# Kernel optimization log

Measured on AMD Instinct MI355X. Metric: run time of the kernel, lower is better.

Reference implementation:

```python
import jax, jax.numpy as jnp
import numpy as np

NEG_INF = -1.0e9  # matches the module's explicit -1e9 masking constant


def setup_inputs() -> dict:
    key = jax.random.key(0)
    B, T, D = 8, 2048, 1024
    x = jax.random.normal(key, (B, T, D), dtype=jnp.float32)
    return {"x": x}


def reference(x):
    # x: [B, T, D]
    T = x.shape[1]
    # raw QK^T scores: [B, T, T]
    scores = jnp.einsum('btd,bsd->bts', x, x)
    # torch.tril(scores, -1) + torch.triu(ones*-1e9, 0):
    # keep strictly-lower entries, set diagonal and upper to -1e9.
    strict_lower = jnp.tril(jnp.ones((T, T), dtype=bool), k=-1)
    scores = jnp.where(strict_lower, scores, jnp.float32(NEG_INF))
    # NOTE: row 0 is all -1e9 -> softmax yields uniform 1/T (faithful to the torch code).
    att_weights = jax.nn.softmax(scores, axis=-1)  # [B, T, T]
    att_vec = jnp.einsum('bts,bsd->btd', att_weights, x)  # [B, T, D]
    return att_vec, att_weights
```

## Files before the change

### kernel.cpp

```cpp
#include <hip/hip_runtime.h>

#define B_ 8
#define T_ 2048
#define D_ 1024

typedef __attribute__((ext_vector_type(8))) short bf16x8;
typedef __attribute__((ext_vector_type(8))) _Float16 f16x8;
typedef __attribute__((ext_vector_type(4))) float f32x4;
typedef __attribute__((ext_vector_type(8))) unsigned short u16x8;
typedef __attribute__((ext_vector_type(4))) unsigned short u16x4;

__device__ __forceinline__ unsigned short f2bf(float f) {
  union { float f; unsigned u; } v; v.f = f;
  unsigned r = v.u + 0x7FFFu + ((v.u >> 16) & 1u);
  return (unsigned short)(r >> 16);
}
__device__ __forceinline__ float bf2f(unsigned short h) {
  union { unsigned u; float f; } v; v.u = ((unsigned)h) << 16; return v.f;
}
__device__ __forceinline__ unsigned short f2h(float f) {
  union { _Float16 h; unsigned short u; } v; v.h = (_Float16)f; return v.u;
}

__device__ __forceinline__ void gl2lds16(const void* g, void* l) {
  __builtin_amdgcn_global_load_lds(
      (__attribute__((address_space(1))) void*)g,
      (__attribute__((address_space(3))) void*)l, 16, 0, 0);
}

__global__ __launch_bounds__(256) void prep_kernel(
    const float* __restrict__ x,
    unsigned short* __restrict__ xh, unsigned short* __restrict__ xl,
    unsigned short* __restrict__ xth) {
  const int b = blockIdx.z;
  const int t0 = blockIdx.y << 6;
  const int d0 = blockIdx.x << 6;
  __shared__ unsigned short tf[64][68];
  const int tid = threadIdx.x;
  const int row = tid & 63, cq = tid >> 6;
  const size_t xoff = ((size_t)b * T_ + t0 + row) * D_ + d0;
#pragma unroll
  for (int c = 0; c < 4; ++c) {
    const int col = (cq << 4) + (c << 2);
    const float4 v = *(const float4*)(x + xoff + col);
    const unsigned short h0 = f2bf(v.x), h1 = f2bf(v.y), h2 = f2bf(v.z), h3 = f2bf(v.w);
    const unsigned short l0 = f2bf(v.x - bf2f(h0)), l1 = f2bf(v.y - bf2f(h1));
    const unsigned short l2 = f2bf(v.z - bf2f(h2)), l3 = f2bf(v.w - bf2f(h3));
    u16x4 hv = {h0, h1, h2, h3}, lv = {l0, l1, l2, l3};
    *(u16x4*)(xh + xoff + col) = hv;
    *(u16x4*)(xl + xoff + col) = lv;
    tf[col + 0][row] = f2h(v.x); tf[col + 1][row] = f2h(v.y);
    tf[col + 2][row] = f2h(v.z); tf[col + 3][row] = f2h(v.w);
  }
  __syncthreads();
  const size_t toff = ((size_t)b * D_ + d0 + row) * T_ + t0;
#pragma unroll
  for (int c = 0; c < 4; ++c) {
    const int col = (cq << 4) + (c << 2);
    *(u16x4*)(xth + toff + col) = *(const u16x4*)&tf[row][col];
  }
}

__global__ __launch_bounds__(256, 4) void scores_mfma(
    const unsigned short* __restrict__ xh, const unsigned short* __restrict__ xl,
    float* __restrict__ w) {
  const int id = blockIdx.x;
  const int sid = ((id & 7) * 136) + (id >> 3);
  const int b = sid / 136;
  const int L = sid - b * 136;
  int tt = (int)((sqrtf(8.f * (float)L + 1.f) - 1.f) * 0.5f);
  while (((tt + 1) * (tt + 2) >> 1) <= L) ++tt;
  while (((tt * (tt + 1)) >> 1) > L) --tt;
  const int ts = L - ((tt * (tt + 1)) >> 1);

  const int t0 = tt << 7, s0 = ts << 7;
  __shared__ unsigned short Ah[128 * 32];
  __shared__ unsigned short Al[128 * 32];
  __shared__ unsigned short Bh[128 * 32];
  __shared__ unsigned short Bl[128 * 32];
  const int tid = threadIdx.x;
  const int lane = tid & 63, wv = tid >> 6;
  const int wr = (wv >> 1) << 6, wc = (wv & 1) << 6;
  const int quad = lane >> 4, r16 = lane & 15;
  const int swz = ((quad ^ (r16 & 3) ^ ((r16 >> 2) & 1)) << 3);
  const size_t xb = (size_t)b * T_ * D_;

  f32x4 acc[4][4];
#pragma unroll
  for (int i = 0; i < 4; ++i)
#pragma unroll
    for (int j = 0; j < 4; ++j) acc[i][j] = (f32x4){0.f, 0.f, 0.f, 0.f};

  for (int k0 = 0; k0 < D_; k0 += 32) {
    __syncthreads();
#pragma unroll
    for (int i = 0; i < 2; ++i) {
      const int cc = (wv << 7) + (i << 6) + lane;
      const int row = cc >> 2, q = cc & 3;
      const int gq = q ^ (row & 3) ^ ((row >> 2) & 1);
      const int ldsoff = (((wv << 7) + (i << 6)) << 3);
      const size_t ga = xb + (size_t)(t0 + row) * D_ + k0 + (gq << 3);
      const size_t gb = xb + (size_t)(s0 + row) * D_ + k0 + (gq << 3);
      gl2lds16(xh + ga, &Ah[ldsoff]);
      gl2lds16(xl + ga, &Al[ldsoff]);
      gl2lds16(xh + gb, &Bh[ldsoff]);
      gl2lds16(xl + gb, &Bl[ldsoff]);
    }
    __syncthreads();
    bf16x8 ah[4], al[4];
#pragma unroll
    for (int i = 0; i < 4; ++i) {
      const int ra = ((wr + (i << 4) + r16) << 5) + swz;
      ah[i] = *(const bf16x8*)&Ah[ra];
      al[i] = *(const bf16x8*)&Al[ra];
    }
#pragma unroll
    for (int j = 0; j < 4; ++j) {
      const int rb = ((wc + (j << 4) + r16) << 5) + swz;
      const bf16x8 bhj = *(const bf16x8*)&Bh[rb];
      const bf16x8 blj = *(const bf16x8*)&Bl[rb];
#pragma unroll
      for (int i = 0; i < 4; ++i)
        acc[i][j] = __builtin_amdgcn_mfma_f32_16x16x32_bf16(ah[i], bhj, acc[i][j], 0, 0, 0);
#pragma unroll
      for (int i = 0; i < 4; ++i)
        acc[i][j] = __builtin_amdgcn_mfma_f32_16x16x32_bf16(ah[i], blj, acc[i][j], 0, 0, 0);
#pragma unroll
      for (int i = 0; i < 4; ++i)
        acc[i][j] = __builtin_amdgcn_mfma_f32_16x16x32_bf16(al[i], bhj, acc[i][j], 0, 0, 0);
    }
  }

  float* wb = w + (size_t)b * T_ * T_;
#pragma unroll
  for (int i = 0; i < 4; ++i)
#pragma unroll
    for (int j = 0; j < 4; ++j) {
      const int rr = t0 + wr + (i << 4) + (quad << 2);
      const int cc = s0 + wc + (j << 4) + r16;
#pragma unroll
      for (int rg = 0; rg < 4; ++rg)
        wb[(size_t)(rr + rg) * T_ + cc] = acc[i][j][rg];
    }
}

template <bool EMIT>
__global__ __launch_bounds__(256) void softmax_kernel(float* __restrict__ w,
                                                      unsigned short* __restrict__ wf) {
  const int row = (blockIdx.x << 2) + (threadIdx.x >> 6);
  const int t = row & (T_ - 1);
  const int lane = threadIdx.x & 63;
  float* wr = w + (size_t)row * T_;
  unsigned short* wfr = wf + (size_t)row * T_;

  if (t == 0) {
    const float u = 1.0f / 2048.0f;
#pragma unroll
    for (int k = 0; k < 32; ++k) {
      wr[lane + (k << 6)] = u;
      if (EMIT && k < 2) wfr[lane + (k << 6)] = 0;
    }
    return;
  }

  const int kmax = ((t >> 7) + 1) << 1;
  float v[32];
  float m = -3.0e38f;
#pragma unroll
  for (int k = 0; k < 32; ++k) {
    const int s = lane + (k << 6);
    float val = -1.0e30f;
    if (s < t) val = wr[s];
    v[k] = val;
    m = fmaxf(m, val);
  }
#pragma unroll
  for (int off = 32; off; off >>= 1) m = fmaxf(m, __shfl_xor(m, off));

  float l = 0.f;
#pragma unroll
  for (int k = 0; k < 32; ++k) {
    v[k] = __expf(v[k] - m);
    l += v[k];
  }
#pragma unroll
  for (int off = 32; off; off >>= 1) l += __shfl_xor(l, off);
  const float inv = 1.0f / l;

#pragma unroll
  for (int k = 0; k < 32; ++k) {
    const float o = v[k] * inv;
    const int s = lane + (k << 6);
    wr[s] = o;
    if (EMIT && k < kmax) wfr[s] = f2h(o);
  }
}

template <bool USE_WF16>
__global__ __launch_bounds__(256, 4) void av_mfma(
    const float* __restrict__ w, const unsigned short* __restrict__ wf,
    const unsigned short* __restrict__ xth, float* __restrict__ out) {
  const int xid = blockIdx.x;
  const int td = xid >> 4;
  const int ti = xid & 15;
  const int tt = (ti < 8) ? ti : (23 - ti);
  const int b = blockIdx.z;
  const int t0 = tt << 7, d0 = td << 7;
  __shared__ unsigned short Aw[128 * 32];
  __shared__ unsigned short Bx[128 * 32];
  const int tid = threadIdx.x;
  const int lane = tid & 63, wv = tid >> 6;
  const int wr = (wv >> 1) << 6, wc = (wv & 1) << 6;
  const int quad = lane >> 4, r16 = lane & 15;
  const int swz = ((quad ^ (r16 & 3) ^ ((r16 >> 2) & 1)) << 3);
  const size_t xtb = (size_t)b * D_ * T_;
  const size_t wbase = (size_t)b * T_ * T_;
  const int smax = t0 + 128;

  f32x4 acc[4][4];
#pragma unroll
  for (int i = 0; i < 4; ++i)
#pragma unroll
    for (int j = 0; j < 4; ++j) acc[i][j] = (f32x4){0.f, 0.f, 0.f, 0.f};

  for (int s0 = 0; s0 < smax; s0 += 32) {
    __syncthreads();
    if (USE_WF16) {
#pragma unroll
      for (int i = 0; i < 2; ++i) {
        const int cc = (wv << 7) + (i << 6) + lane;
        const int row = cc >> 2, q = cc & 3;
        const int gq = q ^ (row & 3) ^ ((row >> 2) & 1);
        const int ldsoff = (((wv << 7) + (i << 6)) << 3);
        gl2lds16(wf + wbase + (size_t)(t0 + row) * T_ + s0 + (gq << 3), &Aw[ldsoff]);
      }
    } else {
      const int row = tid >> 1, half = tid & 1;
      const float* g = w + wbase + (size_t)(t0 + row) * T_ + s0 + (half << 4);
      const float4 v0 = ((const float4*)g)[0];
      const float4 v1 = ((const float4*)g)[1];
      const float4 v2 = ((const float4*)g)[2];
      const float4 v3 = ((const float4*)g)[3];
      const int sw = (row & 3) ^ ((row >> 2) & 1);
      u16x8 p0 = {f2h(v0.x), f2h(v0.y), f2h(v0.z), f2h(v0.w),
                  f2h(v1.x), f2h(v1.y), f2h(v1.z), f2h(v1.w)};
      u16x8 p1 = {f2h(v2.x), f2h(v2.y), f2h(v2.z), f2h(v2.w),
                  f2h(v3.x), f2h(v3.y), f2h(v3.z), f2h(v3.w)};
      *(u16x8*)&Aw[(row << 5) + ((((half << 1) | 0) ^ sw) << 3)] = p0;
      *(u16x8*)&Aw[(row << 5) + ((((half << 1) | 1) ^ sw) << 3)] = p1;
    }
#pragma unroll
    for (int i = 0; i < 2; ++i) {
      const int cc = (wv << 7) + (i << 6) + lane;
      const int row = cc >> 2, q = cc & 3;
      const int gq = q ^ (row & 3) ^ ((row >> 2) & 1);
      const int ldsoff = (((wv << 7) + (i << 6)) << 3);
      gl2lds16(xth + xtb + (size_t)(d0 + row) * T_ + s0 + (gq << 3), &Bx[ldsoff]);
    }
    __syncthreads();
    f16x8 a[4];
#pragma unroll
    for (int i = 0; i < 4; ++i)
      a[i] = *(const f16x8*)&Aw[((wr + (i << 4) + r16) << 5) + swz];
#pragma unroll
    for (int j = 0; j < 4; ++j) {
      const f16x8 bbj = *(const f16x8*)&Bx[((wc + (j << 4) + r16) << 5) + swz];
#pragma unroll
      for (int i = 0; i < 4; ++i)
        acc[i][j] = __builtin_amdgcn_mfma_f32_16x16x32_f16(a[i], bbj, acc[i][j], 0, 0, 0);
    }
  }

  float* ob = out + (size_t)b * T_ * D_;
#pragma unroll
  for (int i = 0; i < 4; ++i)
#pragma unroll
    for (int j = 0; j < 4; ++j) {
      const int rr = t0 + wr + (i << 4) + (quad << 2);
      const int cc = d0 + wc + (j << 4) + r16;
#pragma unroll
      for (int rg = 0; rg < 4; ++rg)
        ob[(size_t)(rr + rg) * D_ + cc] = acc[i][j][rg];
    }
}

__global__ __launch_bounds__(256) void row0_partial(const float* __restrict__ x,
                                                    float* __restrict__ part) {
  const int tc = blockIdx.x, b = blockIdx.y;
  const int tid = threadIdx.x;
  const float* xb = x + ((size_t)b * T_ + (tc << 8)) * D_;
  float4 s = {0.f, 0.f, 0.f, 0.f};
#pragma unroll 4
  for (int r = 0; r < 256; ++r) {
    const float4 v = *(const float4*)(xb + (size_t)r * D_ + (tid << 2));
    s.x += v.x; s.y += v.y; s.z += v.z; s.w += v.w;
  }
  *(float4*)(part + ((size_t)((b << 3) + tc)) * D_ + (tid << 2)) = s;
}

__global__ __launch_bounds__(256) void row0_reduce(const float* __restrict__ part,
                                                   float* __restrict__ out) {
  const int b = blockIdx.x;
  const int tid = threadIdx.x;
  float4 s = {0.f, 0.f, 0.f, 0.f};
#pragma unroll
  for (int p = 0; p < 8; ++p) {
    const float4 v = *(const float4*)(part + ((size_t)((b << 3) + p)) * D_ + (tid << 2));
    s.x += v.x; s.y += v.y; s.z += v.z; s.w += v.w;
  }
  const float sc = 1.0f / 2048.0f;
  float4 o = {s.x * sc, s.y * sc, s.z * sc, s.w * sc};
  *(float4*)(out + (size_t)b * T_ * D_ + (tid << 2)) = o;
}

extern "C" void kernel_launch(void* const* d_in, const int* in_sizes, int n_in,
                              void* d_out, int out_size, void* d_ws, size_t ws_size,
                              hipStream_t stream) {
  const float* x = (const float*)d_in[0];
  float* att_vec = (float*)d_out;
  float* w = (float*)d_out + (size_t)B_ * T_ * D_;

  unsigned short* xh = (unsigned short*)att_vec;
  unsigned short* xl = xh + (size_t)B_ * T_ * D_;
  const size_t xthN = (size_t)B_ * D_ * T_;
  const size_t wfN = (size_t)B_ * T_ * T_;
  unsigned short* xth = (unsigned short*)d_ws;
  unsigned short* wf16 = xth + xthN;
  const size_t need = xthN * 2 + wfN * 2 + (size_t)64 * D_ * 4;
  const bool use_wf16 = (ws_size >= need);
  float* part = use_wf16 ? (float*)(wf16 + wfN) : (float*)(xth + xthN);

  prep_kernel<<<dim3(D_ / 64, T_ / 64, B_), 256, 0, stream>>>(x, xh, xl, xth);
  scores_mfma<<<dim3(8 * 136), 256, 0, stream>>>(xh, xl, w);
  if (use_wf16) {
    softmax_kernel<true><<<dim3(B_ * T_ / 4), 256, 0, stream>>>(w, wf16);
    av_mfma<true><<<dim3(128, 1, B_), 256, 0, stream>>>(w, wf16, xth, att_vec);
  } else {
    softmax_kernel<false><<<dim3(B_ * T_ / 4), 256, 0, stream>>>(w, wf16);
    av_mfma<false><<<dim3(128, 1, B_), 256, 0, stream>>>(w, wf16, xth, att_vec);
  }
  row0_partial<<<dim3(8, B_), 256, 0, stream>>>(x, part);
  row0_reduce<<<dim3(B_), 256, 0, stream>>>(part, att_vec);
}
```

Measured before the change: 538.5 us.

## Vectorize softmax, double AV k-tile to 64, and widen row0 reduction grid

The softmax kernel now loads and stores float4 and half4 vectors per lane instead of scalars, which reduces memory instruction count on the dominant weight traffic. The AV matmul k-tile is doubled from 32 to 64 with a new 8-way XOR swizzle, halving the number of barrier-separated iterations at the cost of more LDS per block. The row-0 mean reduction is split across 64 chunks per batch instead of 8 for more parallelism, and the workspace requirement grows to hold the extra partials.

```diff
diff --git a/kernel.cpp b/kernel.cpp
--- a/kernel.cpp
+++ b/kernel.cpp
@@ -155,44 +155,58 @@
 
   if (t == 0) {
     const float u = 1.0f / 2048.0f;
-#pragma unroll
-    for (int k = 0; k < 32; ++k) {
-      wr[lane + (k << 6)] = u;
-      if (EMIT && k < 2) wfr[lane + (k << 6)] = 0;
+    const float4 uv = {u, u, u, u};
+#pragma unroll
+    for (int k = 0; k < 8; ++k) *(float4*)&wr[(lane << 2) + (k << 8)] = uv;
+    if (EMIT && lane < 32) {
+      u16x4 z = {0, 0, 0, 0};
+      *(u16x4*)&wfr[lane << 2] = z;
     }
     return;
   }
 
-  const int kmax = ((t >> 7) + 1) << 1;
-  float v[32];
+  float4 v[8];
   float m = -3.0e38f;
 #pragma unroll
-  for (int k = 0; k < 32; ++k) {
-    const int s = lane + (k << 6);
-    float val = -1.0e30f;
-    if (s < t) val = wr[s];
+  for (int k = 0; k < 8; ++k) {
+    const int s = (lane << 2) + (k << 8);
+    float4 val = {-1.0e30f, -1.0e30f, -1.0e30f, -1.0e30f};
+    if (s < t) {
+      const float4 g = *(const float4*)&wr[s];
+      val.x = g.x;
+      val.y = (s + 1 < t) ? g.y : -1.0e30f;
+      val.z = (s + 2 < t) ? g.z : -1.0e30f;
+      val.w = (s + 3 < t) ? g.w : -1.0e30f;
+    }
     v[k] = val;
-    m = fmaxf(m, val);
+    m = fmaxf(m, fmaxf(fmaxf(val.x, val.y), fmaxf(val.z, val.w)));
   }
 #pragma unroll
   for (int off = 32; off; off >>= 1) m = fmaxf(m, __shfl_xor(m, off));
 
   float l = 0.f;
 #pragma unroll
-  for (int k = 0; k < 32; ++k) {
-    v[k] = __expf(v[k] - m);
-    l += v[k];
+  for (int k = 0; k < 8; ++k) {
+    v[k].x = __expf(v[k].x - m);
+    v[k].y = __expf(v[k].y - m);
+    v[k].z = __expf(v[k].z - m);
+    v[k].w = __expf(v[k].w - m);
+    l += (v[k].x + v[k].y) + (v[k].z + v[k].w);
   }
 #pragma unroll
   for (int off = 32; off; off >>= 1) l += __shfl_xor(l, off);
   const float inv = 1.0f / l;
 
-#pragma unroll
-  for (int k = 0; k < 32; ++k) {
-    const float o = v[k] * inv;
-    const int s = lane + (k << 6);
-    wr[s] = o;
-    if (EMIT && k < kmax) wfr[s] = f2h(o);
+  const int smax_emit = ((t >> 7) + 1) << 7;
+#pragma unroll
+  for (int k = 0; k < 8; ++k) {
+    const int s = (lane << 2) + (k << 8);
+    const float4 o = {v[k].x * inv, v[k].y * inv, v[k].z * inv, v[k].w * inv};
+    *(float4*)&wr[s] = o;
+    if (EMIT && s < smax_emit) {
+      u16x4 h = {f2h(o.x), f2h(o.y), f2h(o.z), f2h(o.w)};
+      *(u16x4*)&wfr[s] = h;
+    }
   }
 }
 
@@ -206,13 +220,12 @@
   const int tt = (ti < 8) ? ti : (23 - ti);
   const int b = blockIdx.z;
   const int t0 = tt << 7, d0 = td << 7;
-  __shared__ unsigned short Aw[128 * 32];
-  __shared__ unsigned short Bx[128 * 32];
+  __shared__ unsigned short Aw[128 * 64];
+  __shared__ unsigned short Bx[128 * 64];
   const int tid = threadIdx.x;
   const int lane = tid & 63, wv = tid >> 6;
   const int wr = (wv >> 1) << 6, wc = (wv & 1) << 6;
   const int quad = lane >> 4, r16 = lane & 15;
-  const int swz = ((quad ^ (r16 & 3) ^ ((r16 >> 2) & 1)) << 3);
   const size_t xtb = (size_t)b * D_ * T_;
   const size_t wbase = (size_t)b * T_ * T_;
   const int smax = t0 + 128;
@@ -223,51 +236,56 @@
 #pragma unroll
     for (int j = 0; j < 4; ++j) acc[i][j] = (f32x4){0.f, 0.f, 0.f, 0.f};
 
-  for (int s0 = 0; s0 < smax; s0 += 32) {
+  for (int s0 = 0; s0 < smax; s0 += 64) {
     __syncthreads();
     if (USE_WF16) {
 #pragma unroll
-      for (int i = 0; i < 2; ++i) {
-        const int cc = (wv << 7) + (i << 6) + lane;
-        const int row = cc >> 2, q = cc & 3;
-        const int gq = q ^ (row & 3) ^ ((row >> 2) & 1);
-        const int ldsoff = (((wv << 7) + (i << 6)) << 3);
-        gl2lds16(wf + wbase + (size_t)(t0 + row) * T_ + s0 + (gq << 3), &Aw[ldsoff]);
+      for (int i = 0; i < 4; ++i) {
+        const int cc = (wv << 8) + (i << 6) + lane;
+        const int rowa = cc >> 3, q = cc & 7;
+        const int gq = q ^ (rowa & 7);
+        const int ldsoff = (((wv << 8) + (i << 6)) << 3);
+        gl2lds16(wf + wbase + (size_t)(t0 + rowa) * T_ + s0 + (gq << 3), &Aw[ldsoff]);
       }
     } else {
-      const int row = tid >> 1, half = tid & 1;
-      const float* g = w + wbase + (size_t)(t0 + row) * T_ + s0 + (half << 4);
-      const float4 v0 = ((const float4*)g)[0];
-      const float4 v1 = ((const float4*)g)[1];
-      const float4 v2 = ((const float4*)g)[2];
-      const float4 v3 = ((const float4*)g)[3];
-      const int sw = (row & 3) ^ ((row >> 2) & 1);
-      u16x8 p0 = {f2h(v0.x), f2h(v0.y), f2h(v0.z), f2h(v0.w),
-                  f2h(v1.x), f2h(v1.y), f2h(v1.z), f2h(v1.w)};
-      u16x8 p1 = {f2h(v2.x), f2h(v2.y), f2h(v2.z), f2h(v2.w),
-                  f2h(v3.x), f2h(v3.y), f2h(v3.z), f2h(v3.w)};
-      *(u16x8*)&Aw[(row << 5) + ((((half << 1) | 0) ^ sw) << 3)] = p0;
-      *(u16x8*)&Aw[(row << 5) + ((((half << 1) | 1) ^ sw) << 3)] = p1;
-    }
-#pragma unroll
-    for (int i = 0; i < 2; ++i) {
-      const int cc = (wv << 7) + (i << 6) + lane;
-      const int row = cc >> 2, q = cc & 3;
-      const int gq = q ^ (row & 3) ^ ((row >> 2) & 1);
-      const int ldsoff = (((wv << 7) + (i << 6)) << 3);
-      gl2lds16(xth + xtb + (size_t)(d0 + row) * T_ + s0 + (gq << 3), &Bx[ldsoff]);
+      const int rowa = tid >> 1, half = tid & 1;
+      const float* g = w + wbase + (size_t)(t0 + rowa) * T_ + s0 + (half << 5);
+      const int rs = rowa & 7;
+#pragma unroll
+      for (int p = 0; p < 4; ++p) {
+        const float4 va = ((const float4*)g)[2 * p];
+        const float4 vb = ((const float4*)g)[2 * p + 1];
+        u16x8 pk = {f2h(va.x), f2h(va.y), f2h(va.z), f2h(va.w),
+                    f2h(vb.x), f2h(vb.y), f2h(vb.z), f2h(vb.w)};
+        const int c = (half << 2) + p;
+        *(u16x8*)&Aw[(rowa << 6) + ((c ^ rs) << 3)] = pk;
+      }
+    }
+#pragma unroll
+    for (int i = 0; i < 4; ++i) {
+      const int cc = (wv << 8) + (i << 6) + lane;
+      const int rowb = cc >> 3, q = cc & 7;
+      const int gq = q ^ (rowb & 7);
+      const int ldsoff = (((wv << 8) + (i << 6)) << 3);
+      gl2lds16(xth + xtb + (size_t)(d0 + rowb) * T_ + s0 + (gq << 3), &Bx[ldsoff]);
     }
     __syncthreads();
-    f16x8 a[4];
-#pragma unroll
-    for (int i = 0; i < 4; ++i)
-      a[i] = *(const f16x8*)&Aw[((wr + (i << 4) + r16) << 5) + swz];
-#pragma unroll
-    for (int j = 0; j < 4; ++j) {
-      const f16x8 bbj = *(const f16x8*)&Bx[((wc + (j << 4) + r16) << 5) + swz];
-#pragma unroll
-      for (int i = 0; i < 4; ++i)
-        acc[i][j] = __builtin_amdgcn_mfma_f32_16x16x32_f16(a[i], bbj, acc[i][j], 0, 0, 0);
+#pragma unroll
+    for (int h = 0; h < 2; ++h) {
+      f16x8 a[4];
+#pragma unroll
+      for (int i = 0; i < 4; ++i) {
+        const int ar = wr + (i << 4) + r16;
+        a[i] = *(const f16x8*)&Aw[(ar << 6) + ((((h << 2) | quad) ^ (ar & 7)) << 3)];
+      }
+#pragma unroll
+      for (int j = 0; j < 4; ++j) {
+        const int br = wc + (j << 4) + r16;
+        const f16x8 bbj = *(const f16x8*)&Bx[(br << 6) + ((((h << 2) | quad) ^ (br & 7)) << 3)];
+#pragma unroll
+        for (int i = 0; i < 4; ++i)
+          acc[i][j] = __builtin_amdgcn_mfma_f32_16x16x32_f16(a[i], bbj, acc[i][j], 0, 0, 0);
+      }
     }
   }
 
@@ -288,14 +306,14 @@
                                                     float* __restrict__ part) {
   const int tc = blockIdx.x, b = blockIdx.y;
   const int tid = threadIdx.x;
-  const float* xb = x + ((size_t)b * T_ + (tc << 8)) * D_;
+  const float* xb = x + ((size_t)b * T_ + (tc << 5)) * D_;
   float4 s = {0.f, 0.f, 0.f, 0.f};
 #pragma unroll 4
-  for (int r = 0; r < 256; ++r) {
+  for (int r = 0; r < 32; ++r) {
     const float4 v = *(const float4*)(xb + (size_t)r * D_ + (tid << 2));
     s.x += v.x; s.y += v.y; s.z += v.z; s.w += v.w;
   }
-  *(float4*)(part + ((size_t)((b << 3) + tc)) * D_ + (tid << 2)) = s;
+  *(float4*)(part + ((size_t)((b << 6) + tc)) * D_ + (tid << 2)) = s;
 }
 
 __global__ __launch_bounds__(256) void row0_reduce(const float* __restrict__ part,
@@ -303,9 +321,9 @@
   const int b = blockIdx.x;
   const int tid = threadIdx.x;
   float4 s = {0.f, 0.f, 0.f, 0.f};
-#pragma unroll
-  for (int p = 0; p < 8; ++p) {
-    const float4 v = *(const float4*)(part + ((size_t)((b << 3) + p)) * D_ + (tid << 2));
+#pragma unroll 8
+  for (int p = 0; p < 64; ++p) {
+    const float4 v = *(const float4*)(part + ((size_t)((b << 6) + p)) * D_ + (tid << 2));
     s.x += v.x; s.y += v.y; s.z += v.z; s.w += v.w;
   }
   const float sc = 1.0f / 2048.0f;
@@ -326,7 +344,7 @@
   const size_t wfN = (size_t)B_ * T_ * T_;
   unsigned short* xth = (unsigned short*)d_ws;
   unsigned short* wf16 = xth + xthN;
-  const size_t need = xthN * 2 + wfN * 2 + (size_t)64 * D_ * 4;
+  const size_t need = xthN * 2 + wfN * 2 + (size_t)512 * D_ * 4;
   const bool use_wf16 = (ws_size >= need);
   float* part = use_wf16 ? (float*)(wf16 + wfN) : (float*)(xth + xthN);
 
@@ -339,6 +357,6 @@
     softmax_kernel<false><<<dim3(B_ * T_ / 4), 256, 0, stream>>>(w, wf16);
     av_mfma<false><<<dim3(128, 1, B_), 256, 0, stream>>>(w, wf16, xth, att_vec);
   }
-  row0_partial<<<dim3(8, B_), 256, 0, stream>>>(x, part);
+  row0_partial<<<dim3(64, B_), 256, 0, stream>>>(x, part);
   row0_reduce<<<dim3(B_), 256, 0, stream>>>(part, att_vec);
 }
```

New measurement: 509.6 us. -5.4%, faster.
